# Kernel optimization log

Measured on AMD Instinct MI355X. Metric: run time of the kernel, lower is better.

Reference implementation:

```python
import jax, jax.numpy as jnp
import numpy as np

NEG_SLOPE = 0.01  # torch LeakyReLU default
LN_EPS = 1e-5
L2_EPS = 1e-12  # torch F.normalize eps


def setup_inputs() -> dict:
    key = jax.random.key(0)
    ks = jax.random.split(key, 8)
    B, T, N, C = 16, 32, 64, 256
    local_feat = jax.random.normal(ks[0], (B, T, N, C), dtype=jnp.float32)
    global_feat = jax.random.normal(ks[1], (B, C), dtype=jnp.float32)
    pos = jax.random.normal(ks[2], (B, T * N, 3), dtype=jnp.float32)
    adj_w = jax.random.normal(ks[3], (C, C), dtype=jnp.float32) * (1.0 / np.sqrt(C))
    affine_w = jax.random.normal(ks[4], (C, C), dtype=jnp.float32) * np.sqrt(2.0 / C)  # kaiming-ish
    affine_b = jnp.zeros((C,), dtype=jnp.float32)
    ln_g = jnp.ones((C,), dtype=jnp.float32)
    ln_b = jnp.zeros((C,), dtype=jnp.float32)
    return {"local_feat": local_feat, "global_feat": global_feat, "pos": pos,
            "adj_w": adj_w, "affine_w": affine_w, "affine_b": affine_b,
            "ln_g": ln_g, "ln_b": ln_b}


def reference(local_feat, global_feat, pos, adj_w, affine_w, affine_b, ln_g, ln_b):
    B, T, N, C = local_feat.shape
    x = local_feat.reshape(B, T * N, C)  # [B, M, C]
    # L2 normalize along features
    nrm = jnp.sqrt(jnp.sum(x * x, axis=-1, keepdims=True))
    nf = x / jnp.maximum(nrm, L2_EPS)
    # bilinear scores: A = nf @ W @ nf^T  -> [B, M, M]
    A = jnp.einsum('bnc,cd,bmd->bnm', nf, adj_w, nf)
    A = 5.0 * (A - jnp.max(A, axis=-1, keepdims=True))
    A = jax.nn.softmax(A, axis=-1)
    # affine projection (torch Linear: x @ W^T + b)
    h = jnp.einsum('bmc,dc->bmd', x, affine_w) + affine_b
    # aggregation
    h = jnp.einsum('bnm,bmc->bnc', A, h)
    # LayerNorm + LeakyReLU
    mu = jnp.mean(h, axis=-1, keepdims=True)
    var = jnp.mean(jnp.square(h - mu), axis=-1, keepdims=True)
    h = (h - mu) / jnp.sqrt(var + LN_EPS) * ln_g + ln_b
    h = jnp.where(h >= 0, h, NEG_SLOPE * h)
    return h.reshape(B, T, N, C)
```

## Files before the change

### kernel.cpp

```cpp
#include <hip/hip_runtime.h>
#include <hip/hip_bf16.h>
#include <stdint.h>

#define B_  16
#define M_  2048
#define C_  256
#define BM_ 32768

typedef __bf16 bf16x8 __attribute__((ext_vector_type(8)));
typedef __bf16 bf16x2 __attribute__((ext_vector_type(2)));
typedef float  f32x4  __attribute__((ext_vector_type(4)));
typedef float  f32x16 __attribute__((ext_vector_type(16)));
typedef unsigned int uint2v __attribute__((ext_vector_type(2)));

__device__ __forceinline__ unsigned short f2bf(float f) {
    uint32_t u = __builtin_bit_cast(uint32_t, f);
    u += 0x7fffu + ((u >> 16) & 1u);
    return (unsigned short)(u >> 16);
}

__device__ __forceinline__ uint32_t pkbf(float a, float b) {
    bf16x2 t; t[0] = (__bf16)a; t[1] = (__bf16)b;
    return __builtin_bit_cast(uint32_t, t);
}

__device__ __forceinline__ float bf2f(unsigned short u) {
    return __builtin_bit_cast(float, ((uint32_t)u) << 16);
}

__device__ __forceinline__ void gload16(const void* g, void* l) {
    __builtin_amdgcn_global_load_lds(
        (const __attribute__((address_space(1))) void*)g,
        (__attribute__((address_space(3))) void*)l, 16, 0, 0);
}

__device__ __forceinline__ void publish_barrier() {
    asm volatile("s_waitcnt vmcnt(0)" ::: "memory");
    __builtin_amdgcn_sched_barrier(0);
    __syncthreads();
    __builtin_amdgcn_sched_barrier(0);
}

__global__ void prep_weights(const float* __restrict__ adj,
                             const float* __restrict__ affw,
                             unsigned short* __restrict__ adjT5,
                             unsigned short* __restrict__ affwB) {
    int idx = blockIdx.x * 256 + threadIdx.x;
    int d = idx >> 8, c = idx & 255;
    adjT5[d * 256 + c] = f2bf(7.2134752f * adj[c * 256 + d]);
    affwB[idx] = f2bf(affw[idx]);
}

__global__ void l2norm_kernel(const float* __restrict__ x,
                              unsigned short* __restrict__ nf,
                              float* __restrict__ norms) {
    int w = threadIdx.x >> 6, lane = threadIdx.x & 63;
    int row = blockIdx.x * 4 + w;
    const float4 v = *reinterpret_cast<const float4*>(x + (size_t)row * 256 + lane * 4);
    float ss = v.x * v.x + v.y * v.y + v.z * v.z + v.w * v.w;
    #pragma unroll
    for (int m = 1; m < 64; m <<= 1) ss += __shfl_xor(ss, m);
    float nrm = sqrtf(ss);
    float s = 1.0f / fmaxf(nrm, 1e-12f);
    ushort4 o;
    o.x = f2bf(v.x * s); o.y = f2bf(v.y * s); o.z = f2bf(v.z * s); o.w = f2bf(v.w * s);
    *reinterpret_cast<ushort4*>(nf + (size_t)row * 256 + lane * 4) = o;
    if (lane == 0) norms[row] = nrm;
}

__global__ __launch_bounds__(512, 2)
void dual_gemm(const unsigned short* __restrict__ A,
               const unsigned short* __restrict__ B1,
               const unsigned short* __restrict__ B2,
               const float* __restrict__ norms,
               const float* __restrict__ bias,
               unsigned short* __restrict__ outQ,
               unsigned short* __restrict__ outV3,
               unsigned short* __restrict__ outK3) {
    __shared__ unsigned short bb1[256 * 56];
    __shared__ unsigned short bb2[256 * 56];
    int tid = threadIdx.x;
    int w = tid >> 6, lane = tid & 63, g = lane >> 4, r = lane & 15;
    int m0 = blockIdx.x * 128;

    const f32x4 z = {0.f, 0.f, 0.f, 0.f};
    f32x4 accq[16], accv[16];
    #pragma unroll
    for (int i = 0; i < 16; i++) { accq[i] = z; accv[i] = z; }

    int row = m0 + w * 16 + r;
    int kvblk_r = row >> 5, mrow = row & 31;

    for (int dc = 0; dc < 8; dc++) {
        __syncthreads();
        #pragma unroll
        for (int it = 0; it < 2; it++) {
            int n = (w * 2 + it) * 16 + (lane >> 2);
            int t = lane & 3;
            *reinterpret_cast<uint4*>(&bb1[n * 56 + t * 8]) =
                *reinterpret_cast<const uint4*>(B1 + (size_t)n * 256 + dc * 32 + t * 8);
            *reinterpret_cast<uint4*>(&bb2[n * 56 + t * 8]) =
                *reinterpret_cast<const uint4*>(B2 + (size_t)n * 256 + dc * 32 + t * 8);
        }
        __syncthreads();
        bf16x8 af = *reinterpret_cast<const bf16x8*>(
            A + (size_t)row * 256 + dc * 32 + g * 8);
        {
            int ch = dc * 2 + (g >> 1);
            int khl = g & 1;
            *reinterpret_cast<bf16x8*>(
                outK3 + (size_t)kvblk_r * 8192 + ch * 512 + (khl * 32 + mrow) * 8) = af;
        }
        #pragma unroll
        for (int nf16 = 0; nf16 < 16; nf16++) {
            bf16x8 b1f = *reinterpret_cast<const bf16x8*>(&bb1[(nf16 * 16 + r) * 56 + g * 8]);
            accq[nf16] = __builtin_amdgcn_mfma_f32_16x16x32_bf16(af, b1f, accq[nf16], 0, 0, 0);
            bf16x8 b2f = *reinterpret_cast<const bf16x8*>(&bb2[(nf16 * 16 + r) * 56 + g * 8]);
            accv[nf16] = __builtin_amdgcn_mfma_f32_16x16x32_bf16(af, b2f, accv[nf16], 0, 0, 0);
        }
    }
    #pragma unroll
    for (int nf16 = 0; nf16 < 16; nf16++) {
        int n = nf16 * 16 + r;
        #pragma unroll
        for (int j = 0; j < 4; j++) {
            int m = m0 + w * 16 + g * 4 + j;
            outQ[(size_t)m * 256 + n] = f2bf(accq[nf16][j]);
        }
    }
    int mm = m0 + w * 16 + g * 4;
    int kvblk = mm >> 5;
    int kv0 = mm & 31;
    int jj  = kv0 >> 4;
    int hl2 = (kv0 >> 3) & 1;
    int e0  = kv0 & 7;
    float4 nr = *reinterpret_cast<const float4*>(norms + mm);
    #pragma unroll
    for (int nf16 = 0; nf16 < 16; nf16++) {
        int n = nf16 * 16 + r;
        int cb = n >> 5, mr2 = n & 31;
        int slot = (cb * 2 + jj) * 64 + hl2 * 32 + mr2;
        float bv = bias[n];
        ushort4 o;
        o.x = f2bf(accv[nf16][0] * nr.x + bv);
        o.y = f2bf(accv[nf16][1] * nr.y + bv);
        o.z = f2bf(accv[nf16][2] * nr.z + bv);
        o.w = f2bf(accv[nf16][3] * nr.w + bv);
        *reinterpret_cast<ushort4*>(outV3 + (size_t)kvblk * 8192 + slot * 8 + e0) = o;
    }
}

__global__ __launch_bounds__(256, 2)
void flash_kernel(const unsigned short* __restrict__ Q,
                  const unsigned short* __restrict__ K3,
                  const unsigned short* __restrict__ V3,
                  float* __restrict__ out,
                  unsigned short* __restrict__ part0,
                  unsigned short* __restrict__ part1,
                  float* __restrict__ ml,
                  int h0bf16) {
    __shared__ __align__(16) char smem[65536];
    const int tid = threadIdx.x;
    const int w = tid >> 6, lane = tid & 63;
    const int hl = lane >> 5, m = lane & 31;
    const int blk = blockIdx.x;
    const int idx = blk >> 3;
    const int b = (blk & 7) * 2 + (idx >> 5);
    const int sub = idx & 31;
    const int mblk = sub >> 1, h = sub & 1;
    const int q0 = b * M_ + mblk * 128 + w * 32;

    bf16x8 qf[16];
    #pragma unroll
    for (int ch = 0; ch < 16; ch++)
        qf[ch] = *reinterpret_cast<const bf16x8*>(
            Q + (size_t)(q0 + m) * 256 + ch * 16 + hl * 8);

    const f32x16 z16 = {0,0,0,0, 0,0,0,0, 0,0,0,0, 0,0,0,0};
    f32x16 acc[8];
    #pragma unroll
    for (int cb = 0; cb < 8; cb++) acc[cb] = z16;
    float lsum = 0.0f;

    const unsigned short* Ksrc =
        K3 + ((size_t)(b * 64 + h * 32) * 1024 + tid) * 8;
    const unsigned short* Vsrc =
        V3 + ((size_t)(b * 64 + h * 32) * 1024 + tid) * 8;

    auto stageK = [&](int step, int buf) {
        char* kb = smem + buf * 16384;
        const unsigned short* src = Ksrc + (size_t)step * 8192;
        #pragma unroll
        for (int it = 0; it < 4; it++)
            gload16(src + it * 2048, kb + (it * 256 + w * 64) * 16);
    };
    auto stageV = [&](int step, int buf) {
        char* vb = smem + 32768 + buf * 16384;
        const unsigned short* src = Vsrc + (size_t)step * 8192;
        #pragma unroll
        for (int it = 0; it < 4; it++)
            gload16(src + it * 2048, vb + (it * 256 + w * 64) * 16);
    };

    stageK(0, 0); stageV(0, 0);
    publish_barrier();
    stageK(1, 1); stageV(1, 1);

    for (int step = 0; step < 32; step++) {
        const int cur = step & 1;
        const char* kbl = smem + cur * 16384 + lane * 16;
        const char* vbl = smem + 32768 + cur * 16384 + lane * 16;

        f32x16 sf = z16;
        __builtin_amdgcn_s_setprio(1);
        #pragma unroll
        for (int ch = 0; ch < 16; ch++) {
            bf16x8 kf = *reinterpret_cast<const bf16x8*>(kbl + ch * 1024);
            sf = __builtin_amdgcn_mfma_f32_32x32x16_bf16(kf, qf[ch], sf, 0, 0, 0);
        }
        __builtin_amdgcn_s_setprio(0);

        #pragma unroll
        for (int i = 0; i < 16; i++) {
            sf[i] = exp2f(sf[i]);
            lsum += sf[i];
        }
        uint32_t pk0 = pkbf(sf[0], sf[1]),   pk1 = pkbf(sf[2], sf[3]);
        uint32_t pk2 = pkbf(sf[4], sf[5]),   pk3 = pkbf(sf[6], sf[7]);
        uint32_t pk4 = pkbf(sf[8], sf[9]),   pk5 = pkbf(sf[10], sf[11]);
        uint32_t pk6 = pkbf(sf[12], sf[13]), pk7 = pkbf(sf[14], sf[15]);
        uint2v r0 = __builtin_amdgcn_permlane32_swap(pk0, pk2, false, false);
        uint2v r1 = __builtin_amdgcn_permlane32_swap(pk1, pk3, false, false);
        uint2v r2 = __builtin_amdgcn_permlane32_swap(pk4, pk6, false, false);
        uint2v r3 = __builtin_amdgcn_permlane32_swap(pk5, pk7, false, false);
        uint4 u0; u0.x = r0[0]; u0.y = r1[0]; u0.z = r0[1]; u0.w = r1[1];
        uint4 u1; u1.x = r2[0]; u1.y = r3[0]; u1.z = r2[1]; u1.w = r3[1];
        bf16x8 pf0 = __builtin_bit_cast(bf16x8, u0);
        bf16x8 pf1 = __builtin_bit_cast(bf16x8, u1);

        __builtin_amdgcn_s_setprio(1);
        #pragma unroll
        for (int cb = 0; cb < 8; cb++) {
            bf16x8 v0 = *reinterpret_cast<const bf16x8*>(vbl + (cb * 2 + 0) * 1024);
            acc[cb] = __builtin_amdgcn_mfma_f32_32x32x16_bf16(v0, pf0, acc[cb], 0, 0, 0);
            bf16x8 v1 = *reinterpret_cast<const bf16x8*>(vbl + (cb * 2 + 1) * 1024);
            acc[cb] = __builtin_amdgcn_mfma_f32_32x32x16_bf16(v1, pf1, acc[cb], 0, 0, 0);
        }
        __builtin_amdgcn_s_setprio(0);

        publish_barrier();
        if (step + 2 < 32) {
            stageK(step + 2, cur);
            stageV(step + 2, cur);
        }
    }

    lsum += __shfl_xor(lsum, 32);
    float inv = 1.0f / lsum;
    size_t qrow = (size_t)(q0 + m);
    if (h0bf16 || h == 1) {
        unsigned short* myp = h ? part1 : part0;
        #pragma unroll
        for (int cb = 0; cb < 8; cb++)
            #pragma unroll
            for (int q4 = 0; q4 < 4; q4++) {
                int c0i = cb * 32 + q4 * 8 + 4 * hl;
                uint2 u;
                u.x = pkbf(acc[cb][q4 * 4 + 0] * inv, acc[cb][q4 * 4 + 1] * inv);
                u.y = pkbf(acc[cb][q4 * 4 + 2] * inv, acc[cb][q4 * 4 + 3] * inv);
                *reinterpret_cast<uint2*>(myp + qrow * 256 + c0i) = u;
            }
    } else {
        #pragma unroll
        for (int cb = 0; cb < 8; cb++)
            #pragma unroll
            for (int q4 = 0; q4 < 4; q4++) {
                int c0i = cb * 32 + q4 * 8 + 4 * hl;
                float4 o;
                o.x = acc[cb][q4 * 4 + 0] * inv;
                o.y = acc[cb][q4 * 4 + 1] * inv;
                o.z = acc[cb][q4 * 4 + 2] * inv;
                o.w = acc[cb][q4 * 4 + 3] * inv;
                *reinterpret_cast<float4*>(out + qrow * 256 + c0i) = o;
            }
    }
    if (hl == 0) ml[h * BM_ + qrow] = lsum;
}

__global__ void merge_ln_kernel(const unsigned short* __restrict__ part0,
                                const unsigned short* __restrict__ part1,
                                const float* __restrict__ ml,
                                const float* __restrict__ gam,
                                const float* __restrict__ bet,
                                float* __restrict__ out,
                                int h0bf16) {
    int w = threadIdx.x >> 6, lane = threadIdx.x & 63;
    int blk = blockIdx.x;
    int xcd = blk & 7, j = blk >> 3;
    int b = 2 * xcd + (j >> 9);
    size_t row = (size_t)b * 2048 + (size_t)(j & 511) * 4 + w;
    float w0 = ml[row], w1 = ml[BM_ + row];
    float rs = 1.0f / (w0 + w1);
    float a0 = w0 * rs, a1 = w1 * rs;
    float4 v;
    ushort4 p1 = *reinterpret_cast<const ushort4*>(part1 + row * 256 + lane * 4);
    if (h0bf16) {
        ushort4 p0 = *reinterpret_cast<const ushort4*>(part0 + row * 256 + lane * 4);
        v.x = a0 * bf2f(p0.x) + a1 * bf2f(p1.x);
        v.y = a0 * bf2f(p0.y) + a1 * bf2f(p1.y);
        v.z = a0 * bf2f(p0.z) + a1 * bf2f(p1.z);
        v.w = a0 * bf2f(p0.w) + a1 * bf2f(p1.w);
    } else {
        float4 o0 = *reinterpret_cast<float4*>(out + row * 256 + lane * 4);
        v.x = a0 * o0.x + a1 * bf2f(p1.x);
        v.y = a0 * o0.y + a1 * bf2f(p1.y);
        v.z = a0 * o0.z + a1 * bf2f(p1.z);
        v.w = a0 * o0.w + a1 * bf2f(p1.w);
    }
    float s = v.x + v.y + v.z + v.w;
    float q = v.x * v.x + v.y * v.y + v.z * v.z + v.w * v.w;
    #pragma unroll
    for (int m = 1; m < 64; m <<= 1) { s += __shfl_xor(s, m); q += __shfl_xor(q, m); }
    float mu = s * (1.0f / 256.0f);
    float var = q * (1.0f / 256.0f) - mu * mu;
    float rstd = rsqrtf(var + 1e-5f);
    float4 gg = *reinterpret_cast<const float4*>(gam + lane * 4);
    float4 bb = *reinterpret_cast<const float4*>(bet + lane * 4);
    float4 o;
    o.x = (v.x - mu) * rstd * gg.x + bb.x;
    o.y = (v.y - mu) * rstd * gg.y + bb.y;
    o.z = (v.z - mu) * rstd * gg.z + bb.z;
    o.w = (v.w - mu) * rstd * gg.w + bb.w;
    o.x = o.x >= 0.f ? o.x : 0.01f * o.x;
    o.y = o.y >= 0.f ? o.y : 0.01f * o.y;
    o.z = o.z >= 0.f ? o.z : 0.01f * o.z;
    o.w = o.w >= 0.f ? o.w : 0.01f * o.w;
    *reinterpret_cast<float4*>(out + row * 256 + lane * 4) = o;
}

extern "C" void kernel_launch(void* const* d_in, const int* in_sizes, int n_in,
                              void* d_out, int out_size, void* d_ws, size_t ws_size,
                              hipStream_t stream) {
    const float* local_feat = (const float*)d_in[0];
    const float* adj_w    = (const float*)d_in[3];
    const float* affine_w = (const float*)d_in[4];
    const float* affine_b = (const float*)d_in[5];
    const float* ln_g     = (const float*)d_in[6];
    const float* ln_b     = (const float*)d_in[7];
    float* out = (float*)d_out;

    char* ws = (char*)d_ws;
    unsigned short* nf    = (unsigned short*)(ws);
    unsigned short* q     = (unsigned short*)(ws + 16777216);
    unsigned short* v3    = (unsigned short*)(ws + 33554432);
    unsigned short* k3    = (unsigned short*)(ws + 50331648);
    unsigned short* part0 = (unsigned short*)(ws);
    unsigned short* part1;
    unsigned short* adjT5;
    unsigned short* affw;
    float*          norms;
    float*          ml;

    const size_t need = 84279296ull;
    int h0bf16 = (ws_size >= need) ? 1 : 0;
    if (h0bf16) {
        part1 = (unsigned short*)(ws + 67108864);
        adjT5 = (unsigned short*)(ws + 83886080);
        affw  = (unsigned short*)(ws + 84017152);
        norms = (float*)         (ws + 84148224);
        ml    = (float*)         (ws + 83886080);
    } else {
        part1 = (unsigned short*)(ws);
        adjT5 = (unsigned short*)(ws + 67108864);
        affw  = (unsigned short*)(ws + 67239936);
        norms = (float*)         (ws + 67371008);
        ml    = (float*)         (ws + 67108864);
    }

    prep_weights<<<256, 256, 0, stream>>>(adj_w, affine_w, adjT5, affw);
    l2norm_kernel<<<BM_ / 4, 256, 0, stream>>>(local_feat, nf, norms);
    dual_gemm<<<BM_ / 128, 512, 0, stream>>>(nf, adjT5, affw, norms, affine_b, q, v3, k3);
    flash_kernel<<<512, 256, 0, stream>>>(q, k3, v3, out, part0, part1, ml, h0bf16);
    merge_ln_kernel<<<8192, 256, 0, stream>>>(part0, part1, ml, ln_g, ln_b, out, h0bf16);
}
```

Before: 128.7 us.

## Software-pipeline QK softmax ahead of PV with triple-buffered V and fuse prep kernels

The flash kernel now computes the QK^T scores and exp for step s+1 after the PV MFMAs of step s. V gets a third LDS buffer so staging V two steps ahead does not overwrite data still being read, and the single barrier moves to the top of the loop. The aim is to overlap exp and permlane work with matrix ops and cut barrier stalls. The weight-prep kernel is folded into the l2norm kernel as extra blocks to save one launch. LDS per block grows to 80 KB, which can reduce occupancy below the two blocks per CU the launch bounds ask for.

```diff
diff --git a/kernel.cpp b/kernel.cpp
--- a/kernel.cpp
+++ b/kernel.cpp
@@ -41,19 +41,20 @@
     __builtin_amdgcn_sched_barrier(0);
 }
 
-__global__ void prep_weights(const float* __restrict__ adj,
-                             const float* __restrict__ affw,
-                             unsigned short* __restrict__ adjT5,
-                             unsigned short* __restrict__ affwB) {
-    int idx = blockIdx.x * 256 + threadIdx.x;
-    int d = idx >> 8, c = idx & 255;
-    adjT5[d * 256 + c] = f2bf(7.2134752f * adj[c * 256 + d]);
-    affwB[idx] = f2bf(affw[idx]);
-}
-
-__global__ void l2norm_kernel(const float* __restrict__ x,
-                              unsigned short* __restrict__ nf,
-                              float* __restrict__ norms) {
+__global__ void l2norm_prep_kernel(const float* __restrict__ x,
+                                   unsigned short* __restrict__ nf,
+                                   float* __restrict__ norms,
+                                   const float* __restrict__ adj,
+                                   const float* __restrict__ affw,
+                                   unsigned short* __restrict__ adjT5,
+                                   unsigned short* __restrict__ affwB) {
+    if (blockIdx.x >= 8192) {
+        int idx = (blockIdx.x - 8192) * 256 + threadIdx.x;
+        int d = idx >> 8, c = idx & 255;
+        adjT5[d * 256 + c] = f2bf(7.2134752f * adj[c * 256 + d]);
+        affwB[idx] = f2bf(affw[idx]);
+        return;
+    }
     int w = threadIdx.x >> 6, lane = threadIdx.x & 63;
     int row = blockIdx.x * 4 + w;
     const float4 v = *reinterpret_cast<const float4*>(x + (size_t)row * 256 + lane * 4);
@@ -159,7 +160,7 @@
                   unsigned short* __restrict__ part1,
                   float* __restrict__ ml,
                   int h0bf16) {
-    __shared__ __align__(16) char smem[65536];
+    __shared__ __align__(16) char smem[81920];
     const int tid = threadIdx.x;
     const int w = tid >> 6, lane = tid & 63;
     const int hl = lane >> 5, m = lane & 31;
@@ -202,15 +203,9 @@
             gload16(src + it * 2048, vb + (it * 256 + w * 64) * 16);
     };
 
-    stageK(0, 0); stageV(0, 0);
-    publish_barrier();
-    stageK(1, 1); stageV(1, 1);
-
-    for (int step = 0; step < 32; step++) {
-        const int cur = step & 1;
-        const char* kbl = smem + cur * 16384 + lane * 16;
-        const char* vbl = smem + 32768 + cur * 16384 + lane * 16;
-
+    bf16x8 pf0, pf1;
+    auto qksm = [&](int s) {
+        const char* kbl = smem + (s & 1) * 16384 + lane * 16;
         f32x16 sf = z16;
         __builtin_amdgcn_s_setprio(1);
         #pragma unroll
@@ -219,7 +214,6 @@
             sf = __builtin_amdgcn_mfma_f32_32x32x16_bf16(kf, qf[ch], sf, 0, 0, 0);
         }
         __builtin_amdgcn_s_setprio(0);
-
         #pragma unroll
         for (int i = 0; i < 16; i++) {
             sf[i] = exp2f(sf[i]);
@@ -235,24 +229,36 @@
         uint2v r3 = __builtin_amdgcn_permlane32_swap(pk5, pk7, false, false);
         uint4 u0; u0.x = r0[0]; u0.y = r1[0]; u0.z = r0[1]; u0.w = r1[1];
         uint4 u1; u1.x = r2[0]; u1.y = r3[0]; u1.z = r2[1]; u1.w = r3[1];
-        bf16x8 pf0 = __builtin_bit_cast(bf16x8, u0);
-        bf16x8 pf1 = __builtin_bit_cast(bf16x8, u1);
-
+        pf0 = __builtin_bit_cast(bf16x8, u0);
+        pf1 = __builtin_bit_cast(bf16x8, u1);
+    };
+
+    stageK(0, 0); stageV(0, 0);
+    publish_barrier();
+    stageK(1, 1); stageV(1, 1);
+    qksm(0);
+
+    int vcur = 0;
+    for (int s = 0; s < 32; s++) {
+        publish_barrier();
+        if (s + 2 < 32) {
+            int vst = vcur + 2; if (vst >= 3) vst -= 3;
+            stageK(s + 2, s & 1);
+            stageV(s + 2, vst);
+        }
+        const char* vbl = smem + 32768 + vcur * 16384 + lane * 16;
+        bf16x8 p0 = pf0, p1 = pf1;
         __builtin_amdgcn_s_setprio(1);
         #pragma unroll
         for (int cb = 0; cb < 8; cb++) {
             bf16x8 v0 = *reinterpret_cast<const bf16x8*>(vbl + (cb * 2 + 0) * 1024);
-            acc[cb] = __builtin_amdgcn_mfma_f32_32x32x16_bf16(v0, pf0, acc[cb], 0, 0, 0);
+            acc[cb] = __builtin_amdgcn_mfma_f32_32x32x16_bf16(v0, p0, acc[cb], 0, 0, 0);
             bf16x8 v1 = *reinterpret_cast<const bf16x8*>(vbl + (cb * 2 + 1) * 1024);
-            acc[cb] = __builtin_amdgcn_mfma_f32_32x32x16_bf16(v1, pf1, acc[cb], 0, 0, 0);
+            acc[cb] = __builtin_amdgcn_mfma_f32_32x32x16_bf16(v1, p1, acc[cb], 0, 0, 0);
         }
         __builtin_amdgcn_s_setprio(0);
-
-        publish_barrier();
-        if (step + 2 < 32) {
-            stageK(step + 2, cur);
-            stageV(step + 2, cur);
-        }
+        if (s + 1 < 32) qksm(s + 1);
+        vcur++; if (vcur >= 3) vcur -= 3;
     }
 
     lsum += __shfl_xor(lsum, 32);
@@ -377,8 +383,8 @@
         ml    = (float*)         (ws + 67108864);
     }
 
-    prep_weights<<<256, 256, 0, stream>>>(adj_w, affine_w, adjT5, affw);
-    l2norm_kernel<<<BM_ / 4, 256, 0, stream>>>(local_feat, nf, norms);
+    l2norm_prep_kernel<<<8448, 256, 0, stream>>>(local_feat, nf, norms,
+                                                 adj_w, affine_w, adjT5, affw);
     dual_gemm<<<BM_ / 128, 512, 0, stream>>>(nf, adjT5, affw, norms, affine_b, q, v3, k3);
     flash_kernel<<<512, 256, 0, stream>>>(q, k3, v3, out, part0, part1, ml, h0bf16);
     merge_ln_kernel<<<8192, 256, 0, stream>>>(part0, part1, ml, ln_g, ln_b, out, h0bf16);
```

Result: faster. 124.5 us (-3.3%).
